# Kernel optimization log

Measured on AMD Instinct MI355X. Metric: run time of the kernel, lower is better.

The kernel has to match this reference:

```python
import jax, jax.numpy as jnp
import numpy as np

E = 8       # expert_number
TOP_K = 2


def setup_inputs() -> dict:
    key = jax.random.key(0)
    ks = jax.random.split(key, 5)
    B, S, D, H = 4, 2048, 1024, 4096
    scale = 0.02
    return {
        "x": jax.random.normal(ks[0], (B, S, D), dtype=jnp.float32),
        "gate_w": jax.random.normal(ks[1], (D, E), dtype=jnp.float32) * scale,
        "gate_b": jnp.zeros((E,), dtype=jnp.float32),
        "w1": jax.random.normal(ks[2], (E, D, H), dtype=jnp.float32) * scale,
        "b1": jnp.zeros((E, H), dtype=jnp.float32),
        "w2": jax.random.normal(ks[3], (E, H, D), dtype=jnp.float32) * scale,
        "b2": jnp.zeros((E, D), dtype=jnp.float32),
    }


def reference(x, gate_w, gate_b, w1, b1, w2, b2):
    B, S, D = x.shape
    h = x.reshape(-1, D)                                   # [T, D]

    # Router: softmax in fp32, top-k, renormalize (matches torch code)
    router_logits = h @ gate_w + gate_b                    # [T, E]
    probs = jax.nn.softmax(router_logits.astype(jnp.float32), axis=-1)
    rw, sel = jax.lax.top_k(probs, TOP_K)                  # [T, K] each
    rw = rw / rw.sum(axis=-1, keepdims=True)
    rw = rw.astype(h.dtype)

    # Per-token combine weight for each expert (0 if not selected): [T, E]
    we = (jax.nn.one_hot(sel, E, dtype=h.dtype) * rw[..., None]).sum(axis=1)

    out = jnp.zeros_like(h)
    for e in range(E):  # fixed small expert count; per-expert GEMM + weighted combine
        mid = jax.nn.gelu(h @ w1[e] + b1[e], approximate=False)  # [T, H]
        ye = mid @ w2[e] + b2[e]                                 # [T, D]
        out = out + we[:, e:e + 1] * ye

    return out.reshape(B, S, D), router_logits
```

## Files before the change

kernel.cpp:

```cpp
#include <hip/hip_runtime.h>
#include <hip/hip_bf16.h>
#include <math.h>

#define T_TOKENS 8192
#define DDIM 1024
#define HDIM 4096
#define NEXP 8
#define CAP 8192
#define MAXTILES 136

typedef __bf16 bf16;
typedef __bf16 bf16x2 __attribute__((ext_vector_type(2)));
typedef __bf16 bf16x4 __attribute__((ext_vector_type(4)));
typedef __bf16 bf16x8 __attribute__((ext_vector_type(8)));
typedef float  floatx4 __attribute__((ext_vector_type(4)));

__device__ static inline void async_load16(const void* g, void* l)
{
    __builtin_amdgcn_global_load_lds(
        (const __attribute__((address_space(1))) void*)g,
        (__attribute__((address_space(3))) void*)l, 16, 0, 0);
}

__global__ void router_kernel(const float* __restrict__ x,
                              const float* __restrict__ gw,
                              const float* __restrict__ gbias,
                              float* __restrict__ logits_out,
                              int* counts, int* token_of,
                              int* selpack, int* slots, float* wts)
{
    int t = blockIdx.x;
    int l = threadIdx.x;
    const float4* xr = (const float4*)(x + (size_t)t * DDIM);

    float p[NEXP];
#pragma unroll
    for (int e = 0; e < NEXP; ++e) p[e] = 0.f;

#pragma unroll
    for (int it = 0; it < 4; ++it) {
        int d4 = it * 64 + l;
        float4 v = xr[d4];
        float vv[4] = {v.x, v.y, v.z, v.w};
#pragma unroll
        for (int j = 0; j < 4; ++j) {
            const float4* g4 = (const float4*)(gw + (size_t)(d4 * 4 + j) * NEXP);
            float4 ga = g4[0], gb4 = g4[1];
            p[0] += vv[j] * ga.x;  p[1] += vv[j] * ga.y;
            p[2] += vv[j] * ga.z;  p[3] += vv[j] * ga.w;
            p[4] += vv[j] * gb4.x; p[5] += vv[j] * gb4.y;
            p[6] += vv[j] * gb4.z; p[7] += vv[j] * gb4.w;
        }
    }
#pragma unroll
    for (int e = 0; e < NEXP; ++e) {
#pragma unroll
        for (int off = 32; off; off >>= 1) p[e] += __shfl_xor(p[e], off);
        p[e] += gbias[e];
    }
    if (l < NEXP) logits_out[(size_t)t * NEXP + l] = p[l];

    if (l == 0) {
        int e0 = 0;
#pragma unroll
        for (int e = 1; e < NEXP; ++e) if (p[e] > p[e0]) e0 = e;
        int e1 = -1;
#pragma unroll
        for (int e = 0; e < NEXP; ++e) {
            if (e == e0) continue;
            if (e1 < 0 || p[e] > p[e1]) e1 = e;
        }
        float w0 = 1.f / (1.f + expf(p[e1] - p[e0]));
        float w1 = 1.f / (1.f + expf(p[e0] - p[e1]));
        int s0 = atomicAdd(&counts[e0], 1);
        int s1 = atomicAdd(&counts[e1], 1);
        token_of[e0 * CAP + s0] = t;
        token_of[e1 * CAP + s1] = t;
        selpack[t] = e0 | (e1 << 8);
        slots[2 * t]     = s0;
        slots[2 * t + 1] = s1;
        wts[2 * t]     = w0;
        wts[2 * t + 1] = w1;
    }
}

__global__ void offsets_kernel(const int* __restrict__ counts,
                               int* __restrict__ offsets,
                               int* __restrict__ tiles,
                               int* __restrict__ ntiles)
{
    if (threadIdx.x == 0) {
        int a = 0, nt = 0;
        for (int e = 0; e < NEXP; ++e) {
            offsets[e] = a;
            for (int r = 0; r < counts[e]; r += 128)
                tiles[nt++] = (e << 24) | (a + r);
            a += counts[e];
        }
        offsets[NEXP] = a;
        *ntiles = nt;
    }
}

__global__ void gather_kernel(const float* __restrict__ x,
                              const int* __restrict__ offsets,
                              const int* __restrict__ token_of,
                              bf16* __restrict__ xg)
{
    int row = blockIdx.x * 4 + (threadIdx.x >> 6);
    int l = threadIdx.x & 63;
    int e = 0;
#pragma unroll
    for (int i = 1; i < NEXP; ++i) e += (row >= offsets[i]);
    int t = token_of[e * CAP + (row - offsets[e])];
    const float4* src = (const float4*)(x + (size_t)t * DDIM);
    bf16x4* dst = (bf16x4*)(xg + (size_t)row * DDIM);
#pragma unroll
    for (int it = 0; it < 4; ++it) {
        float4 v = src[it * 64 + l];
        bf16x4 b;
        b[0] = (bf16)v.x; b[1] = (bf16)v.y; b[2] = (bf16)v.z; b[3] = (bf16)v.w;
        dst[it * 64 + l] = b;
    }
}

__global__ void transpose_cvt_kernel(const float* __restrict__ in,
                                     bf16* __restrict__ out, int R, int C)
{
    __shared__ bf16 tile[64][68];
    int e = blockIdx.z;
    const float* src = in + (size_t)e * R * C;
    bf16* dst = out + (size_t)e * R * C;
    int r0 = blockIdx.y * 64, c0 = blockIdx.x * 64;
    int t = threadIdx.x;
    int lr = t >> 4, c4 = t & 15;
#pragma unroll
    for (int it = 0; it < 4; ++it) {
        int r = lr + it * 16;
        float4 v = *(const float4*)(src + (size_t)(r0 + r) * C + c0 + c4 * 4);
        bf16x4 b;
        b[0] = (bf16)v.x; b[1] = (bf16)v.y; b[2] = (bf16)v.z; b[3] = (bf16)v.w;
        *(bf16x4*)(&tile[r][c4 * 4]) = b;
    }
    __syncthreads();
    int oc = t >> 3, rseg = (t & 7) * 8;
#pragma unroll
    for (int it = 0; it < 2; ++it) {
        int c = oc + it * 32;
        bf16x8 v;
#pragma unroll
        for (int j = 0; j < 8; ++j) v[j] = tile[rseg + j][c];
        *(bf16x8*)(dst + (size_t)(c0 + c) * R + r0 + rseg) = v;
    }
}

template<int KTOT>
__device__ static inline void stage_tile(const bf16* __restrict__ gbase,
                                         bf16* lds, int wave, int lane, int valid)
{
#pragma unroll
    for (int it = 0; it < 4; ++it) {
        int rbase = wave * 32 + it * 8;
        int rloc  = rbase + (lane >> 3);
        int grow  = rloc < valid ? rloc : (valid - 1);
        int chunk = (lane & 7) ^ (rloc & 7);
        const bf16* g = gbase + (size_t)grow * KTOT + chunk * 8;
        async_load16(g, lds + rbase * 64);
    }
}

__device__ static inline float fast_gelu(float v)
{
    float z = v * (2.302236479f + 0.1029451170f * v * v);
    float ex = __builtin_amdgcn_exp2f(z);
    return v * ex * __builtin_amdgcn_rcpf(ex + 1.f);
}

template<int KTOT, int NTOT, bool DOGELU, typename OutT>
__global__ __launch_bounds__(256, 4)
void moe_gemm(const bf16* __restrict__ Abase, const bf16* __restrict__ Bbase,
              const float* __restrict__ bias, OutT* __restrict__ Out,
              const int* __restrict__ tiles, const int* __restrict__ ntiles,
              const int* __restrict__ offsets)
{
    if (blockIdx.x >= *ntiles) return;
    int info = tiles[blockIdx.x];
    int e = info >> 24, row0 = info & 0xffffff;
    int valid = offsets[e + 1] - row0; if (valid > 128) valid = 128;
    int n0 = blockIdx.y * 128;

    const bf16* A = Abase + (size_t)row0 * KTOT;
    const bf16* B = Bbase + (size_t)e * NTOT * KTOT + (size_t)n0 * KTOT;
    const float* bvec = bias + (size_t)e * NTOT + n0;

    __shared__ __align__(16) bf16 As[128 * 64];
    __shared__ __align__(16) bf16 Bs[128 * 64];

    int tid = threadIdx.x;
    int lane = tid & 63, wave = tid >> 6;
    int wr = wave >> 1, wc = wave & 1;
    int m16 = lane & 15, quad = lane >> 4;
    int swz = m16 & 7;

    floatx4 acc[4][4];
#pragma unroll
    for (int i = 0; i < 4; ++i)
#pragma unroll
        for (int j = 0; j < 4; ++j)
#pragma unroll
            for (int r = 0; r < 4; ++r) acc[i][j][r] = 0.f;

    for (int k0 = 0; k0 < KTOT; k0 += 64) {
        stage_tile<KTOT>(A + k0, As, wave, lane, valid);
        stage_tile<KTOT>(B + k0, Bs, wave, lane, 128);
        __syncthreads();
#pragma unroll
        for (int ks = 0; ks < 64; ks += 32) {
            int cbase = (ks >> 3) + quad;
            int pchunk = (cbase ^ swz) * 8;
            bf16x8 af[4], bfr[4];
#pragma unroll
            for (int i = 0; i < 4; ++i)
                af[i] = *(const bf16x8*)(&As[(wr * 64 + i * 16 + m16) * 64 + pchunk]);
#pragma unroll
            for (int j = 0; j < 4; ++j)
                bfr[j] = *(const bf16x8*)(&Bs[(wc * 64 + j * 16 + m16) * 64 + pchunk]);
#pragma unroll
            for (int i = 0; i < 4; ++i)
#pragma unroll
                for (int j = 0; j < 4; ++j)
                    acc[i][j] = __builtin_amdgcn_mfma_f32_16x16x32_bf16(
                        af[i], bfr[j], acc[i][j], 0, 0, 0);
        }
        __syncthreads();
    }

#pragma unroll
    for (int i = 0; i < 4; ++i) {
#pragma unroll
        for (int r = 0; r < 4; ++r) {
            int lrow = wr * 64 + i * 16 + quad * 4 + r;
            if (lrow >= valid) continue;
            size_t orow = (size_t)(row0 + lrow) * NTOT + n0;
#pragma unroll
            for (int j = 0; j < 4; ++j) {
                int lcol = wc * 64 + j * 16 + m16;
                float v = acc[i][j][r] + bvec[lcol];
                if (DOGELU) v = fast_gelu(v);
                Out[orow + lcol] = (OutT)v;
            }
        }
    }
}

__global__ void combine_kernel(const float* __restrict__ y,
                               const int* __restrict__ offsets,
                               const int* __restrict__ selpack,
                               const int* __restrict__ slots,
                               const float* __restrict__ wts,
                               float* __restrict__ out)
{
    int t = blockIdx.x;
    int sp = selpack[t];
    int e0 = sp & 0xff, e1 = (sp >> 8) & 0xff;
    int p0 = offsets[e0] + slots[2 * t];
    int p1 = offsets[e1] + slots[2 * t + 1];
    float w0 = wts[2 * t], w1 = wts[2 * t + 1];
    const float4* y0 = (const float4*)(y + (size_t)p0 * DDIM);
    const float4* y1 = (const float4*)(y + (size_t)p1 * DDIM);
    float4* o = (float4*)(out + (size_t)t * DDIM);
    int tid = threadIdx.x;
    float4 a = y0[tid], b = y1[tid];
    float4 rr;
    rr.x = w0 * a.x + w1 * b.x;
    rr.y = w0 * a.y + w1 * b.y;
    rr.z = w0 * a.z + w1 * b.z;
    rr.w = w0 * a.w + w1 * b.w;
    o[tid] = rr;
}

extern "C" void kernel_launch(void* const* d_in, const int* in_sizes, int n_in,
                              void* d_out, int out_size, void* d_ws, size_t ws_size,
                              hipStream_t stream)
{
    (void)in_sizes; (void)n_in; (void)out_size; (void)ws_size;
    const float* x  = (const float*)d_in[0];
    const float* gw = (const float*)d_in[1];
    const float* gb = (const float*)d_in[2];
    const float* w1 = (const float*)d_in[3];
    const float* b1 = (const float*)d_in[4];
    const float* w2 = (const float*)d_in[5];
    const float* b2 = (const float*)d_in[6];
    float* out    = (float*)d_out;
    float* logits = out + (size_t)T_TOKENS * DDIM;

    char* ws = (char*)d_ws;
    const size_t MB = 1024 * 1024;
    int*   counts   = (int*)(ws + 0);
    int*   offsets  = (int*)(ws + 256);
    int*   tiles    = (int*)(ws + 512);
    int*   ntiles   = (int*)(ws + 512 + 1024);
    int*   selpack  = (int*)(ws + 4096);
    int*   slots    = (int*)(ws + 4096 + 32 * 1024);
    float* wts      = (float*)(ws + 4096 + 96 * 1024);
    int*   token_of = (int*)(ws + 4096 + 160 * 1024);
    bf16*  xg  = (bf16*)(ws + 1 * MB);
    bf16*  w1b = (bf16*)(ws + 33 * MB);
    bf16*  w2b = (bf16*)(ws + 97 * MB);
    bf16*  mid = (bf16*)(ws + 161 * MB);
    float* y   = (float*)(ws + 289 * MB);

    hipMemsetAsync(counts, 0, 32, stream);

    router_kernel<<<T_TOKENS, 64, 0, stream>>>(x, gw, gb, logits, counts,
                                               token_of, selpack, slots, wts);
    offsets_kernel<<<1, 64, 0, stream>>>(counts, offsets, tiles, ntiles);
    gather_kernel<<<2 * T_TOKENS / 4, 256, 0, stream>>>(x, offsets, token_of, xg);
    transpose_cvt_kernel<<<dim3(HDIM / 64, DDIM / 64, NEXP), 256, 0, stream>>>(
        w1, w1b, DDIM, HDIM);
    transpose_cvt_kernel<<<dim3(DDIM / 64, HDIM / 64, NEXP), 256, 0, stream>>>(
        w2, w2b, HDIM, DDIM);
    moe_gemm<DDIM, HDIM, true, bf16><<<dim3(MAXTILES, HDIM / 128), 256, 0, stream>>>(
        xg, w1b, b1, mid, tiles, ntiles, offsets);
    moe_gemm<HDIM, DDIM, false, float><<<dim3(MAXTILES, DDIM / 128), 256, 0, stream>>>(
        mid, w2b, b2, y, tiles, ntiles, offsets);
    combine_kernel<<<T_TOKENS, 256, 0, stream>>>(y, offsets, selpack, slots, wts, out);
}
```

Before: 970.5 us.

## Interleave MoE tile list across XCDs, fuse weight transposes, batch router tokens

The tile list is rearranged so each group of blocks sharing blockIdx.x mod 8 gets a contiguous run of tiles, padded with -1 entries that early-exit. On a chiplet GPU that dispatches blocks round-robin, this aims to keep one expert's weights local to one cache domain and balance the tiles. The two weight transpose launches are merged into one grid, and the router processes four tokens per 256-thread block to cut launch and block overhead. Padding blocks still launch and read the tile list.

```diff
diff --git a/kernel.cpp b/kernel.cpp
--- a/kernel.cpp
+++ b/kernel.cpp
@@ -10,7 +10,6 @@
 #define MAXTILES 136
 
 typedef __bf16 bf16;
-typedef __bf16 bf16x2 __attribute__((ext_vector_type(2)));
 typedef __bf16 bf16x4 __attribute__((ext_vector_type(4)));
 typedef __bf16 bf16x8 __attribute__((ext_vector_type(8)));
 typedef float  floatx4 __attribute__((ext_vector_type(4)));
@@ -29,8 +28,8 @@
                               int* counts, int* token_of,
                               int* selpack, int* slots, float* wts)
 {
-    int t = blockIdx.x;
-    int l = threadIdx.x;
+    int t = blockIdx.x * 4 + (threadIdx.x >> 6);
+    int l = threadIdx.x & 63;
     const float4* xr = (const float4*)(x + (size_t)t * DDIM);
 
     float p[NEXP];
@@ -86,19 +85,24 @@
 
 __global__ void offsets_kernel(const int* __restrict__ counts,
                                int* __restrict__ offsets,
-                               int* __restrict__ tiles,
-                               int* __restrict__ ntiles)
+                               int* __restrict__ tiles)
 {
     if (threadIdx.x == 0) {
+        int tmp[MAXTILES];
         int a = 0, nt = 0;
         for (int e = 0; e < NEXP; ++e) {
             offsets[e] = a;
             for (int r = 0; r < counts[e]; r += 128)
-                tiles[nt++] = (e << 24) | (a + r);
+                tmp[nt++] = (e << 24) | (a + r);
             a += counts[e];
         }
         offsets[NEXP] = a;
-        *ntiles = nt;
+        int per = (nt + 7) >> 3;
+        for (int p = 0; p < MAXTILES; ++p) {
+            int c = p & 7, k = p >> 3;
+            int src = c * per + k;
+            tiles[p] = (k < per && src < nt) ? tmp[src] : -1;
+        }
     }
 }
 
@@ -124,23 +128,38 @@
     }
 }
 
-__global__ void transpose_cvt_kernel(const float* __restrict__ in,
-                                     bf16* __restrict__ out, int R, int C)
+__global__ void transpose_cvt_kernel(const float* __restrict__ w1,
+                                     const float* __restrict__ w2,
+                                     bf16* __restrict__ w1b,
+                                     bf16* __restrict__ w2b)
 {
     __shared__ bf16 tile[64][68];
-    int e = blockIdx.z;
-    const float* src = in + (size_t)e * R * C;
-    bf16* dst = out + (size_t)e * R * C;
-    int r0 = blockIdx.y * 64, c0 = blockIdx.x * 64;
+    int b = blockIdx.x;
+    int R, C, e, tr, tc;
+    const float* src;
+    bf16* dst;
+    if (b < 8192) {
+        R = DDIM; C = HDIM;
+        e = b >> 10; int tt = b & 1023;
+        tc = tt & 63; tr = tt >> 6;
+        src = w1 + (size_t)e * R * C; dst = w1b + (size_t)e * R * C;
+    } else {
+        b -= 8192;
+        R = HDIM; C = DDIM;
+        e = b >> 10; int tt = b & 1023;
+        tc = tt & 15; tr = tt >> 4;
+        src = w2 + (size_t)e * R * C; dst = w2b + (size_t)e * R * C;
+    }
+    int r0 = tr * 64, c0 = tc * 64;
     int t = threadIdx.x;
     int lr = t >> 4, c4 = t & 15;
 #pragma unroll
     for (int it = 0; it < 4; ++it) {
         int r = lr + it * 16;
         float4 v = *(const float4*)(src + (size_t)(r0 + r) * C + c0 + c4 * 4);
-        bf16x4 b;
-        b[0] = (bf16)v.x; b[1] = (bf16)v.y; b[2] = (bf16)v.z; b[3] = (bf16)v.w;
-        *(bf16x4*)(&tile[r][c4 * 4]) = b;
+        bf16x4 bb;
+        bb[0] = (bf16)v.x; bb[1] = (bf16)v.y; bb[2] = (bf16)v.z; bb[3] = (bf16)v.w;
+        *(bf16x4*)(&tile[r][c4 * 4]) = bb;
     }
     __syncthreads();
     int oc = t >> 3, rseg = (t & 7) * 8;
@@ -180,11 +199,10 @@
 __global__ __launch_bounds__(256, 4)
 void moe_gemm(const bf16* __restrict__ Abase, const bf16* __restrict__ Bbase,
               const float* __restrict__ bias, OutT* __restrict__ Out,
-              const int* __restrict__ tiles, const int* __restrict__ ntiles,
-              const int* __restrict__ offsets)
-{
-    if (blockIdx.x >= *ntiles) return;
+              const int* __restrict__ tiles, const int* __restrict__ offsets)
+{
     int info = tiles[blockIdx.x];
+    if (info < 0) return;
     int e = info >> 24, row0 = info & 0xffffff;
     int valid = offsets[e + 1] - row0; if (valid > 128) valid = 128;
     int n0 = blockIdx.y * 128;
@@ -299,7 +317,6 @@
     int*   counts   = (int*)(ws + 0);
     int*   offsets  = (int*)(ws + 256);
     int*   tiles    = (int*)(ws + 512);
-    int*   ntiles   = (int*)(ws + 512 + 1024);
     int*   selpack  = (int*)(ws + 4096);
     int*   slots    = (int*)(ws + 4096 + 32 * 1024);
     float* wts      = (float*)(ws + 4096 + 96 * 1024);
@@ -312,17 +329,14 @@
 
     hipMemsetAsync(counts, 0, 32, stream);
 
-    router_kernel<<<T_TOKENS, 64, 0, stream>>>(x, gw, gb, logits, counts,
-                                               token_of, selpack, slots, wts);
-    offsets_kernel<<<1, 64, 0, stream>>>(counts, offsets, tiles, ntiles);
+    router_kernel<<<T_TOKENS / 4, 256, 0, stream>>>(x, gw, gb, logits, counts,
+                                                    token_of, selpack, slots, wts);
+    offsets_kernel<<<1, 64, 0, stream>>>(counts, offsets, tiles);
     gather_kernel<<<2 * T_TOKENS / 4, 256, 0, stream>>>(x, offsets, token_of, xg);
-    transpose_cvt_kernel<<<dim3(HDIM / 64, DDIM / 64, NEXP), 256, 0, stream>>>(
-        w1, w1b, DDIM, HDIM);
-    transpose_cvt_kernel<<<dim3(DDIM / 64, HDIM / 64, NEXP), 256, 0, stream>>>(
-        w2, w2b, HDIM, DDIM);
+    transpose_cvt_kernel<<<16384, 256, 0, stream>>>(w1, w2, w1b, w2b);
     moe_gemm<DDIM, HDIM, true, bf16><<<dim3(MAXTILES, HDIM / 128), 256, 0, stream>>>(
-        xg, w1b, b1, mid, tiles, ntiles, offsets);
+        xg, w1b, b1, mid, tiles, offsets);
     moe_gemm<HDIM, DDIM, false, float><<<dim3(MAXTILES, DDIM / 128), 256, 0, stream>>>(
-        mid, w2b, b2, y, tiles, ntiles, offsets);
+        mid, w2b, b2, y, tiles, offsets);
     combine_kernel<<<T_TOKENS, 256, 0, stream>>>(y, offsets, selpack, slots, wts, out);
 }
```

Result: no change. 961.8 us (-0.9%).
